# Performance work log

Hardware: AMD Instinct MI355X
Metric: run time of the kernel (lower is better)

## Reference

```python
import jax, jax.numpy as jnp
import numpy as np
import math

B, Q_LEN, PAST, HID = 1, 1024, 3072, 4096
NH, NKV, HD = 32, 8, 128
KV_LEN = PAST + Q_LEN
ROPE_THETA = 10000.0


def setup_inputs() -> dict:
    key = jax.random.key(0)
    ks = jax.random.split(key, 8)
    s = 0.02
    hidden_states = jax.random.normal(ks[0], (B, Q_LEN, HID), jnp.float32)
    # additive causal mask with KV cache offset: query i attends keys j <= PAST + i
    i = jnp.arange(Q_LEN)[:, None]
    j = jnp.arange(KV_LEN)[None, :]
    attention_mask = jnp.where(j <= PAST + i, 0.0, -1e9).astype(jnp.float32)[None, None]
    position_ids = (jnp.arange(Q_LEN, dtype=jnp.int64) + PAST)[None, :]
    past_k = jax.random.normal(ks[1], (B, NKV, PAST, HD), jnp.float32)
    past_v = jax.random.normal(ks[2], (B, NKV, PAST, HD), jnp.float32)
    Wq = jax.random.normal(ks[3], (NH * HD, HID), jnp.float32) * s
    Wk = jax.random.normal(ks[4], (NKV * HD, HID), jnp.float32) * s
    Wv = jax.random.normal(ks[5], (NKV * HD, HID), jnp.float32) * s
    Wo = jax.random.normal(ks[6], (HID, NH * HD), jnp.float32) * s
    return {"hidden_states": hidden_states, "attention_mask": attention_mask,
            "position_ids": position_ids, "past_k": past_k, "past_v": past_v,
            "Wq": Wq, "Wk": Wk, "Wv": Wv, "Wo": Wo}


def _rope_tables(seq_len, head_dim, dtype):
    inv_freq = 1.0 / (ROPE_THETA ** (jnp.arange(0, head_dim, 2, dtype=jnp.float32) / head_dim))
    t = jnp.arange(seq_len, dtype=jnp.float32)
    freqs = jnp.outer(t, inv_freq)            # [seq, hd/2]
    emb = jnp.concatenate([freqs, freqs], -1)  # [seq, hd]
    return jnp.cos(emb).astype(dtype), jnp.sin(emb).astype(dtype)


def _rotate_half(x):
    x1, x2 = jnp.split(x, 2, axis=-1)
    return jnp.concatenate([-x2, x1], axis=-1)


def reference(hidden_states, attention_mask, position_ids, past_k, past_v, Wq, Wk, Wv, Wo):
    bsz, q_len, _ = hidden_states.shape
    q = (hidden_states @ Wq.T).reshape(bsz, q_len, NH, HD).transpose(0, 2, 1, 3)
    k = (hidden_states @ Wk.T).reshape(bsz, q_len, NKV, HD).transpose(0, 2, 1, 3)
    v = (hidden_states @ Wv.T).reshape(bsz, q_len, NKV, HD).transpose(0, 2, 1, 3)

    kv_seq_len = q_len + past_k.shape[2]
    cos_t, sin_t = _rope_tables(kv_seq_len, HD, q.dtype)
    cos = cos_t[position_ids][:, None]  # [b,1,q,hd]
    sin = sin_t[position_ids][:, None]
    q = q * cos + _rotate_half(q) * sin
    k = k * cos + _rotate_half(k) * sin

    k = jnp.concatenate([past_k, k], axis=2)  # [b,nkv,kv,hd]
    v = jnp.concatenate([past_v, v], axis=2)
    n_rep = NH // NKV
    k = jnp.repeat(k, n_rep, axis=1)  # GQA repeat_kv -> [b,nh,kv,hd]
    v = jnp.repeat(v, n_rep, axis=1)

    scores = jnp.einsum('bhqd,bhkd->bhqk', q, k) / math.sqrt(HD)
    scores = scores + attention_mask
    weights = jax.nn.softmax(scores.astype(jnp.float32), axis=-1).astype(q.dtype)
    attn = jnp.einsum('bhqk,bhkd->bhqd', weights, v)
    attn = attn.transpose(0, 2, 1, 3).reshape(bsz, q_len, NH * HD)
    return attn @ Wo.T
```

## Files before the change

### kernel.cpp

```cpp
#include <hip/hip_runtime.h>

#define QLEN 1024
#define PASTN 3072
#define KVLEN 4096
#define HIDN 4096
#define NHEAD 32
#define NKVH 8
#define HDIM 128
#define NQKVC 6144

typedef unsigned short u16;
typedef __bf16 bf16x8 __attribute__((ext_vector_type(8)));
typedef float f32x4 __attribute__((ext_vector_type(4)));
typedef u16 us8 __attribute__((ext_vector_type(8)));
typedef u16 us4 __attribute__((ext_vector_type(4)));

__device__ __forceinline__ u16 f2bf(float x) {
  unsigned u = __builtin_bit_cast(unsigned, x);
  u += 0x7fffu + ((u >> 16) & 1u);
  return (u16)(u >> 16);
}
__device__ __forceinline__ float bf2f(u16 b) {
  return __builtin_bit_cast(float, (unsigned)b << 16);
}

#define GLL16(gp, lp) __builtin_amdgcn_global_load_lds( \
    (const __attribute__((address_space(1))) void*)(gp), \
    (__attribute__((address_space(3))) void*)(lp), 16, 0, 0)

__global__ __launch_bounds__(256) void cvt_kernel(const float* __restrict__ src,
                                                  u16* __restrict__ dst, int n) {
  int i = (blockIdx.x * 256 + threadIdx.x) * 4;
  if (i >= n) return;
  float4 f = *(const float4*)(src + i);
  ushort4 o = make_ushort4(f2bf(f.x), f2bf(f.y), f2bf(f.z), f2bf(f.w));
  *(ushort4*)(dst + i) = o;
}

__device__ __forceinline__ void storeC(float* p, float v) { *p = v; }
__device__ __forceinline__ void storeC(u16* p, float v) { *p = f2bf(v); }

template <typename CT>
__global__ __launch_bounds__(256) void gemm_bt(const u16* __restrict__ A,
                                               const u16* __restrict__ B,
                                               CT* __restrict__ C, int M, int N, int K) {
  __shared__ u16 Alds[2][128 * 32];
  __shared__ u16 Blds[2][128 * 32];
  const int tid = threadIdx.x, wid = tid >> 6, lane = tid & 63;
  const int m0 = blockIdx.y * 128, n0 = blockIdx.x * 128;
  const int wm = (wid >> 1) * 64, wn = (wid & 1) * 64;
  const int l15 = lane & 15, l4 = lane >> 4;
  const int srow = lane >> 2, scol = (lane & 3) * 8;
  f32x4 acc[4][4] = {};
  auto stage = [&](int buf, int kt) {
#pragma unroll
    for (int i = 0; i < 2; ++i) {
      int c = wid * 2 + i;
      GLL16(A + (size_t)(m0 + c * 16 + srow) * K + kt + scol, &Alds[buf][c * 512]);
      GLL16(B + (size_t)(n0 + c * 16 + srow) * K + kt + scol, &Blds[buf][c * 512]);
    }
  };
  stage(0, 0);
  __syncthreads();
  int cur = 0;
  for (int kt = 0; kt < K; kt += 32) {
    if (kt + 32 < K) stage(cur ^ 1, kt + 32);
    bf16x8 a[4], b[4];
#pragma unroll
    for (int i = 0; i < 4; ++i) {
      a[i] = *(const bf16x8*)&Alds[cur][(wm + i * 16 + l15) * 32 + l4 * 8];
      b[i] = *(const bf16x8*)&Blds[cur][(wn + i * 16 + l15) * 32 + l4 * 8];
    }
#pragma unroll
    for (int i = 0; i < 4; ++i)
#pragma unroll
      for (int j = 0; j < 4; ++j)
        acc[i][j] = __builtin_amdgcn_mfma_f32_16x16x32_bf16(a[i], b[j], acc[i][j], 0, 0, 0);
    __syncthreads();
    cur ^= 1;
  }
#pragma unroll
  for (int i = 0; i < 4; ++i)
#pragma unroll
    for (int j = 0; j < 4; ++j) {
      int row = m0 + wm + i * 16 + l4 * 4;
      int col = n0 + wn + j * 16 + l15;
#pragma unroll
      for (int r = 0; r < 4; ++r) storeC(&C[(size_t)(row + r) * N + col], acc[i][j][r]);
    }
}

__global__ __launch_bounds__(256) void rope_q_kernel(const u16* __restrict__ qkv,
                                                     u16* __restrict__ qr) {
  int idx = blockIdx.x * 256 + threadIdx.x;
  int i = idx & 63, h = (idx >> 6) & 31, r = idx >> 11;
  float freq = __expf(-(float)i * (9.210340371976184f / 64.f));
  float angle = (float)(PASTN + r) * freq;
  float sn, cs;
  sincosf(angle, &sn, &cs);
  int base = r * NQKVC + h * HDIM + i;
  float x1 = bf2f(qkv[base]);
  float x2 = bf2f(qkv[base + 64]);
  int ob = r * HIDN + h * HDIM + i;
  qr[ob] = f2bf(x1 * cs - x2 * sn);
  qr[ob + 64] = f2bf(x2 * cs + x1 * sn);
}

__global__ __launch_bounds__(256) void repack_k_kernel(const float* __restrict__ past_k,
                                                       const u16* __restrict__ qkv,
                                                       u16* __restrict__ kb) {
  int idx = blockIdx.x * 256 + threadIdx.x;
  int d = idx & 127, kv = (idx >> 7) & 4095, hk = idx >> 19;
  float val;
  if (kv < PASTN) {
    val = past_k[((size_t)hk * PASTN + kv) * HDIM + d];
  } else {
    int r = kv - PASTN;
    float x = bf2f(qkv[(size_t)r * NQKVC + 4096 + hk * HDIM + d]);
    float xp = bf2f(qkv[(size_t)r * NQKVC + 4096 + hk * HDIM + (d ^ 64)]);
    int i = d & 63;
    float freq = __expf(-(float)i * (9.210340371976184f / 64.f));
    float angle = (float)(PASTN + r) * freq;
    float sn, cs;
    sincosf(angle, &sn, &cs);
    val = (d < 64) ? (x * cs - xp * sn) : (x * cs + xp * sn);
  }
  kb[idx] = f2bf(val);
}

__global__ __launch_bounds__(256) void repack_vt_kernel(const float* __restrict__ past_v,
                                                        const u16* __restrict__ qkv,
                                                        u16* __restrict__ vtb) {
  __shared__ u16 tile[32][136];
  int hk = blockIdx.y, kv0 = blockIdx.x * 32, tid = threadIdx.x;
  int j = tid >> 3, d0 = (tid & 7) * 16;
  if (kv0 < PASTN) {
    const float* src = past_v + ((size_t)hk * PASTN + kv0 + j) * HDIM + d0;
#pragma unroll
    for (int x = 0; x < 16; x += 4) {
      float4 f = *(const float4*)(src + x);
      tile[j][d0 + x] = f2bf(f.x);
      tile[j][d0 + x + 1] = f2bf(f.y);
      tile[j][d0 + x + 2] = f2bf(f.z);
      tile[j][d0 + x + 3] = f2bf(f.w);
    }
  } else {
    int r = kv0 - PASTN + j;
    const u16* src = qkv + (size_t)r * NQKVC + 5120 + hk * HDIM + d0;
    *(us8*)&tile[j][d0] = *(const us8*)src;
    *(us8*)&tile[j][d0 + 8] = *(const us8*)(src + 8);
  }
  __syncthreads();
  int d = tid >> 1, jb = (tid & 1) * 16;
  us8 o0, o1;
#pragma unroll
  for (int x = 0; x < 8; ++x) {
    o0[x] = tile[jb + x][d];
    o1[x] = tile[jb + 8 + x][d];
  }
  u16* dst = vtb + ((size_t)hk * HDIM + d) * KVLEN + kv0 + jb;
  *(us8*)dst = o0;
  *(us8*)(dst + 8) = o1;
}

__global__ __launch_bounds__(256) void attn_kernel(const u16* __restrict__ q,
                                                   const u16* __restrict__ kc,
                                                   const u16* __restrict__ vt,
                                                   u16* __restrict__ o) {
  __shared__ u16 Klds[2][64 * 128];
  __shared__ u16 Vlds[2][128 * 64];
  const int tid = threadIdx.x, wid = tid >> 6, lane = tid & 63;
  const int l15 = lane & 15, l4 = lane >> 4;
  const int h = blockIdx.y, hk = h >> 2;
  const int q0 = blockIdx.x * 64;
  bf16x8 qf[4];
  {
    const u16* qp = q + (size_t)(q0 + wid * 16 + l15) * HIDN + h * HDIM + l4 * 8;
#pragma unroll
    for (int dk = 0; dk < 4; ++dk) qf[dk] = *(const bf16x8*)(qp + dk * 32);
  }
  float m_run = -1e30f, l_run = 0.f;
  f32x4 oacc[8] = {};
  const u16* kbase = kc + (size_t)hk * KVLEN * HDIM;
  const u16* vbase = vt + (size_t)hk * HDIM * KVLEN;
  const int ntiles = (PASTN + q0 + 64) >> 6;
  const float C = 0.12753102f;
  const int qpos = PASTN + q0 + wid * 16 + l15;
  auto stage = [&](int buf, int kv0) {
#pragma unroll
    for (int i = 0; i < 4; ++i) {
      const int base = (wid * 4 + i) * 512;
      const int row = (wid * 4 + i) * 4 + l4;
      const int kap = (row & 0x23) | ((row & 0x0C) << 1) | ((row & 0x10) >> 2);
      const int col = l15 ^ (row & 7);
      GLL16(kbase + (size_t)(kv0 + kap) * HDIM + col * 8, &Klds[buf][base]);
    }
#pragma unroll
    for (int i = 0; i < 4; ++i) {
      const int base = (wid * 4 + i) * 512;
      const int d = (wid * 4 + i) * 8 + (lane >> 3);
      const int kvo = ((lane & 7) ^ (d & 7)) * 8;
      GLL16(vbase + (size_t)d * KVLEN + kv0 + kvo, &Vlds[buf][base]);
    }
  };
  stage(0, 0);
  __syncthreads();
  int cur = 0;
  for (int t = 0; t < ntiles; ++t) {
    if (t + 1 < ntiles) stage(cur ^ 1, (t + 1) << 6);
    const int kv0 = t << 6;
    const u16* Kb = Klds[cur];
    const u16* Vb = Vlds[cur];
    f32x4 s[4];
    __builtin_amdgcn_s_setprio(1);
#pragma unroll
    for (int kj = 0; kj < 4; ++kj) {
      s[kj] = f32x4{0.f, 0.f, 0.f, 0.f};
#pragma unroll
      for (int dk = 0; dk < 4; ++dk) {
        const int idx = (kj * 16 + l15) * 128 + ((dk * 32 + l4 * 8) ^ ((l15 & 7) << 3));
        bf16x8 kf = *(const bf16x8*)&Kb[idx];
        s[kj] = __builtin_amdgcn_mfma_f32_16x16x32_bf16(kf, qf[dk], s[kj], 0, 0, 0);
      }
    }
    __builtin_amdgcn_s_setprio(0);
    float pm = -1e30f;
    if (t == ntiles - 1) {
#pragma unroll
      for (int kj = 0; kj < 4; ++kj) {
        const int kb = kv0 + ((kj >> 1) << 5) + l4 * 8 + ((kj & 1) << 2);
#pragma unroll
        for (int r = 0; r < 4; ++r) {
          float v = s[kj][r] * C;
          if (kb + r > qpos) v = -1e30f;
          s[kj][r] = v;
          pm = fmaxf(pm, v);
        }
      }
    } else {
#pragma unroll
      for (int kj = 0; kj < 4; ++kj)
#pragma unroll
        for (int r = 0; r < 4; ++r) {
          float v = s[kj][r] * C;
          s[kj][r] = v;
          pm = fmaxf(pm, v);
        }
    }
    pm = fmaxf(pm, __shfl_xor(pm, 16));
    pm = fmaxf(pm, __shfl_xor(pm, 32));
    if (!__all(pm <= m_run)) {
      const float mn = fmaxf(m_run, pm);
      const float corr = exp2f(m_run - mn);
      m_run = mn;
      l_run *= corr;
#pragma unroll
      for (int di = 0; di < 8; ++di)
#pragma unroll
        for (int r = 0; r < 4; ++r) oacc[di][r] *= corr;
    }
    float rs = 0.f;
#pragma unroll
    for (int kj = 0; kj < 4; ++kj)
#pragma unroll
      for (int r = 0; r < 4; ++r) {
        const float p = exp2f(s[kj][r] - m_run);
        s[kj][r] = p;
        rs += p;
      }
    rs += __shfl_xor(rs, 16);
    rs += __shfl_xor(rs, 32);
    l_run += rs;
    __builtin_amdgcn_s_setprio(1);
#pragma unroll
    for (int b = 0; b < 2; ++b) {
      bf16x8 pa;
#pragma unroll
      for (int r = 0; r < 4; ++r) {
        pa[r] = (__bf16)s[2 * b][r];
        pa[4 + r] = (__bf16)s[2 * b + 1][r];
      }
#pragma unroll
      for (int di = 0; di < 8; ++di) {
        const int d = di * 16 + l15;
        const int idx = d * 64 + ((b * 32 + l4 * 8) ^ ((d & 7) << 3));
        bf16x8 vf = *(const bf16x8*)&Vb[idx];
        oacc[di] = __builtin_amdgcn_mfma_f32_16x16x32_bf16(vf, pa, oacc[di], 0, 0, 0);
      }
    }
    __builtin_amdgcn_s_setprio(0);
    __syncthreads();
    cur ^= 1;
  }
  const float inv = 1.f / l_run;
  u16* Kb0 = Klds[0];
#pragma unroll
  for (int di = 0; di < 8; ++di) {
    us4 w4;
#pragma unroll
    for (int r = 0; r < 4; ++r) w4[r] = f2bf(oacc[di][r] * inv);
    const int row = wid * 16 + l15;
    *(us4*)&Kb0[row * 128 + ((di * 16 + l4 * 4) ^ ((l15 & 7) << 3))] = w4;
  }
  __syncthreads();
  {
    const int row = tid >> 2, c0 = (tid & 3) * 32;
    u16* dst = o + (size_t)(q0 + row) * HIDN + h * HDIM + c0;
#pragma unroll
    for (int x = 0; x < 4; ++x)
      *(us8*)(dst + x * 8) =
          *(const us8*)&Kb0[row * 128 + ((c0 + x * 8) ^ ((row & 7) << 3))];
  }
}

extern "C" void kernel_launch(void* const* d_in, const int* in_sizes, int n_in,
                              void* d_out, int out_size, void* d_ws, size_t ws_size,
                              hipStream_t stream) {
  (void)in_sizes; (void)n_in; (void)out_size; (void)ws_size;
  const float* hidden = (const float*)d_in[0];
  const float* past_k = (const float*)d_in[3];
  const float* past_v = (const float*)d_in[4];
  const float* Wq = (const float*)d_in[5];
  const float* Wk = (const float*)d_in[6];
  const float* Wv = (const float*)d_in[7];
  const float* Wo = (const float*)d_in[8];
  float* out = (float*)d_out;

  char* w = (char*)d_ws;
  u16* hiddenb = (u16*)w; w += (size_t)QLEN * HIDN * 2;
  u16* wqkv    = (u16*)w; w += (size_t)NQKVC * HIDN * 2;
  u16* wo      = (u16*)w; w += (size_t)HIDN * HIDN * 2;
  u16* qkvraw  = (u16*)w; w += (size_t)QLEN * NQKVC * 2;
  u16* qrope   = (u16*)w; w += (size_t)QLEN * HIDN * 2;
  u16* kbuf    = (u16*)w; w += (size_t)NKVH * KVLEN * HDIM * 2;
  u16* vtbuf   = (u16*)w; w += (size_t)NKVH * HDIM * KVLEN * 2;
  u16* attnb   = (u16*)w; w += (size_t)QLEN * HIDN * 2;

  cvt_kernel<<<(QLEN * HIDN) / 1024, 256, 0, stream>>>(hidden, hiddenb, QLEN * HIDN);
  cvt_kernel<<<(NHEAD * HDIM * HIDN) / 1024, 256, 0, stream>>>(Wq, wqkv, NHEAD * HDIM * HIDN);
  cvt_kernel<<<(NKVH * HDIM * HIDN) / 1024, 256, 0, stream>>>(Wk, wqkv + (size_t)4096 * HIDN,
                                                              NKVH * HDIM * HIDN);
  cvt_kernel<<<(NKVH * HDIM * HIDN) / 1024, 256, 0, stream>>>(Wv, wqkv + (size_t)5120 * HIDN,
                                                              NKVH * HDIM * HIDN);
  cvt_kernel<<<(HIDN * HIDN) / 1024, 256, 0, stream>>>(Wo, wo, HIDN * HIDN);

  gemm_bt<u16><<<dim3(NQKVC / 128, QLEN / 128), 256, 0, stream>>>(hiddenb, wqkv, qkvraw,
                                                                  QLEN, NQKVC, HIDN);

  rope_q_kernel<<<(QLEN * NHEAD * 64) / 256, 256, 0, stream>>>(qkvraw, qrope);
  repack_k_kernel<<<(NKVH * KVLEN * HDIM) / 256, 256, 0, stream>>>(past_k, qkvraw, kbuf);
  repack_vt_kernel<<<dim3(KVLEN / 32, NKVH), 256, 0, stream>>>(past_v, qkvraw, vtbuf);

  attn_kernel<<<dim3(QLEN / 64, NHEAD), 256, 0, stream>>>(qrope, kbuf, vtbuf, attnb);

  gemm_bt<float><<<dim3(HIDN / 128, QLEN / 128), 256, 0, stream>>>(attnb, wo, out,
                                                                   QLEN, HIDN, HIDN);
}
```

Before: 375.6 us.

## Switch attention to 32x32x16 MFMA with two waves per 64-query block

The attention kernel now uses 32x32x16 bf16 MFMA instructions instead of 16x16x32, so each wave owns 32 query rows, and the block shrinks from four waves to two (128 threads). The LDS swizzle for K and V staging and for the output tile is redone to fit the new fragment layouts, and one cross-lane shuffle step in the softmax reductions goes away. The aim is fewer LDS fragment reads per FLOP and fewer MFMA issues. In exchange, each block has half as many waves to hide latency, each thread issues twice as many staging loads, and register pressure per thread is higher.

```diff
diff --git a/kernel.cpp b/kernel.cpp
--- a/kernel.cpp
+++ b/kernel.cpp
@@ -12,6 +12,7 @@
 typedef unsigned short u16;
 typedef __bf16 bf16x8 __attribute__((ext_vector_type(8)));
 typedef float f32x4 __attribute__((ext_vector_type(4)));
+typedef float f32x16 __attribute__((ext_vector_type(16)));
 typedef u16 us8 __attribute__((ext_vector_type(8)));
 typedef u16 us4 __attribute__((ext_vector_type(4)));
 
@@ -163,44 +164,45 @@
   *(us8*)(dst + 8) = o1;
 }
 
-__global__ __launch_bounds__(256) void attn_kernel(const u16* __restrict__ q,
+__global__ __launch_bounds__(128) void attn_kernel(const u16* __restrict__ q,
                                                    const u16* __restrict__ kc,
                                                    const u16* __restrict__ vt,
                                                    u16* __restrict__ o) {
   __shared__ u16 Klds[2][64 * 128];
   __shared__ u16 Vlds[2][128 * 64];
   const int tid = threadIdx.x, wid = tid >> 6, lane = tid & 63;
-  const int l15 = lane & 15, l4 = lane >> 4;
+  const int l31 = lane & 31, hi = lane >> 5, l15 = lane & 15;
   const int h = blockIdx.y, hk = h >> 2;
   const int q0 = blockIdx.x * 64;
-  bf16x8 qf[4];
+  const int qrow = q0 + wid * 32 + l31;
+  bf16x8 qf[8];
   {
-    const u16* qp = q + (size_t)(q0 + wid * 16 + l15) * HIDN + h * HDIM + l4 * 8;
-#pragma unroll
-    for (int dk = 0; dk < 4; ++dk) qf[dk] = *(const bf16x8*)(qp + dk * 32);
+    const u16* qp = q + (size_t)qrow * HIDN + h * HDIM + hi * 8;
+#pragma unroll
+    for (int dk = 0; dk < 8; ++dk) qf[dk] = *(const bf16x8*)(qp + dk * 16);
   }
   float m_run = -1e30f, l_run = 0.f;
-  f32x4 oacc[8] = {};
+  f32x16 oacc[4] = {};
   const u16* kbase = kc + (size_t)hk * KVLEN * HDIM;
   const u16* vbase = vt + (size_t)hk * HDIM * KVLEN;
   const int ntiles = (PASTN + q0 + 64) >> 6;
   const float C = 0.12753102f;
-  const int qpos = PASTN + q0 + wid * 16 + l15;
+  const int qpos = PASTN + qrow;
   auto stage = [&](int buf, int kv0) {
 #pragma unroll
-    for (int i = 0; i < 4; ++i) {
-      const int base = (wid * 4 + i) * 512;
-      const int row = (wid * 4 + i) * 4 + l4;
-      const int kap = (row & 0x23) | ((row & 0x0C) << 1) | ((row & 0x10) >> 2);
-      const int col = l15 ^ (row & 7);
-      GLL16(kbase + (size_t)(kv0 + kap) * HDIM + col * 8, &Klds[buf][base]);
-    }
-#pragma unroll
-    for (int i = 0; i < 4; ++i) {
-      const int base = (wid * 4 + i) * 512;
-      const int d = (wid * 4 + i) * 8 + (lane >> 3);
-      const int kvo = ((lane & 7) ^ (d & 7)) * 8;
-      GLL16(vbase + (size_t)d * KVLEN + kv0 + kvo, &Vlds[buf][base]);
+    for (int i = 0; i < 8; ++i) {
+      const int w = wid * 8 + i;
+      const int p = w * 4 + (lane >> 4);
+      const int key = (p & 0x33) | ((p & 4) << 1) | ((p & 8) >> 1);
+      const int sl = (lane & 15) ^ (p & 15);
+      GLL16(kbase + (size_t)(kv0 + key) * HDIM + sl * 8, &Klds[buf][w * 512]);
+    }
+#pragma unroll
+    for (int i = 0; i < 8; ++i) {
+      const int w = wid * 8 + i;
+      const int d = w * 8 + (lane >> 3);
+      const int sl = (lane & 7) ^ ((lane >> 3) & 7);
+      GLL16(vbase + (size_t)d * KVLEN + kv0 + sl * 8, &Vlds[buf][w * 512]);
     }
   };
   stage(0, 0);
@@ -211,43 +213,39 @@
     const int kv0 = t << 6;
     const u16* Kb = Klds[cur];
     const u16* Vb = Vlds[cur];
-    f32x4 s[4];
+    f32x16 s[2] = {};
     __builtin_amdgcn_s_setprio(1);
 #pragma unroll
-    for (int kj = 0; kj < 4; ++kj) {
-      s[kj] = f32x4{0.f, 0.f, 0.f, 0.f};
-#pragma unroll
-      for (int dk = 0; dk < 4; ++dk) {
-        const int idx = (kj * 16 + l15) * 128 + ((dk * 32 + l4 * 8) ^ ((l15 & 7) << 3));
+    for (int tt = 0; tt < 2; ++tt)
+#pragma unroll
+      for (int dk = 0; dk < 8; ++dk) {
+        const int idx = (tt * 32 + l31) * 128 + (((dk * 2 + hi) ^ l15) * 8);
         bf16x8 kf = *(const bf16x8*)&Kb[idx];
-        s[kj] = __builtin_amdgcn_mfma_f32_16x16x32_bf16(kf, qf[dk], s[kj], 0, 0, 0);
+        s[tt] = __builtin_amdgcn_mfma_f32_32x32x16_bf16(kf, qf[dk], s[tt], 0, 0, 0);
       }
-    }
     __builtin_amdgcn_s_setprio(0);
     float pm = -1e30f;
     if (t == ntiles - 1) {
 #pragma unroll
-      for (int kj = 0; kj < 4; ++kj) {
-        const int kb = kv0 + ((kj >> 1) << 5) + l4 * 8 + ((kj & 1) << 2);
-#pragma unroll
-        for (int r = 0; r < 4; ++r) {
-          float v = s[kj][r] * C;
-          if (kb + r > qpos) v = -1e30f;
-          s[kj][r] = v;
+      for (int tt = 0; tt < 2; ++tt)
+#pragma unroll
+        for (int reg = 0; reg < 16; ++reg) {
+          const int key = kv0 + tt * 32 + (reg & 7) + 8 * hi + ((reg & 8) << 1);
+          float v = s[tt][reg] * C;
+          if (key > qpos) v = -1e30f;
+          s[tt][reg] = v;
           pm = fmaxf(pm, v);
         }
-      }
     } else {
 #pragma unroll
-      for (int kj = 0; kj < 4; ++kj)
-#pragma unroll
-        for (int r = 0; r < 4; ++r) {
-          float v = s[kj][r] * C;
-          s[kj][r] = v;
+      for (int tt = 0; tt < 2; ++tt)
+#pragma unroll
+        for (int reg = 0; reg < 16; ++reg) {
+          float v = s[tt][reg] * C;
+          s[tt][reg] = v;
           pm = fmaxf(pm, v);
         }
     }
-    pm = fmaxf(pm, __shfl_xor(pm, 16));
     pm = fmaxf(pm, __shfl_xor(pm, 32));
     if (!__all(pm <= m_run)) {
       const float mn = fmaxf(m_run, pm);
@@ -255,37 +253,32 @@
       m_run = mn;
       l_run *= corr;
 #pragma unroll
-      for (int di = 0; di < 8; ++di)
-#pragma unroll
-        for (int r = 0; r < 4; ++r) oacc[di][r] *= corr;
+      for (int db = 0; db < 4; ++db)
+#pragma unroll
+        for (int r = 0; r < 16; ++r) oacc[db][r] *= corr;
     }
     float rs = 0.f;
 #pragma unroll
-    for (int kj = 0; kj < 4; ++kj)
-#pragma unroll
-      for (int r = 0; r < 4; ++r) {
-        const float p = exp2f(s[kj][r] - m_run);
-        s[kj][r] = p;
+    for (int tt = 0; tt < 2; ++tt)
+#pragma unroll
+      for (int reg = 0; reg < 16; ++reg) {
+        const float p = exp2f(s[tt][reg] - m_run);
+        s[tt][reg] = p;
         rs += p;
       }
-    rs += __shfl_xor(rs, 16);
     rs += __shfl_xor(rs, 32);
     l_run += rs;
     __builtin_amdgcn_s_setprio(1);
 #pragma unroll
-    for (int b = 0; b < 2; ++b) {
+    for (int kc2 = 0; kc2 < 4; ++kc2) {
       bf16x8 pa;
 #pragma unroll
-      for (int r = 0; r < 4; ++r) {
-        pa[r] = (__bf16)s[2 * b][r];
-        pa[4 + r] = (__bf16)s[2 * b + 1][r];
-      }
-#pragma unroll
-      for (int di = 0; di < 8; ++di) {
-        const int d = di * 16 + l15;
-        const int idx = d * 64 + ((b * 32 + l4 * 8) ^ ((d & 7) << 3));
+      for (int j = 0; j < 8; ++j) pa[j] = (__bf16)s[kc2 >> 1][(kc2 & 1) * 8 + j];
+#pragma unroll
+      for (int db = 0; db < 4; ++db) {
+        const int idx = (db * 32 + l31) * 64 + (((kc2 * 2 + hi) ^ (l31 & 7)) * 8);
         bf16x8 vf = *(const bf16x8*)&Vb[idx];
-        oacc[di] = __builtin_amdgcn_mfma_f32_16x16x32_bf16(vf, pa, oacc[di], 0, 0, 0);
+        oacc[db] = __builtin_amdgcn_mfma_f32_32x32x16_bf16(vf, pa, oacc[db], 0, 0, 0);
       }
     }
     __builtin_amdgcn_s_setprio(0);
@@ -293,23 +286,25 @@
     cur ^= 1;
   }
   const float inv = 1.f / l_run;
-  u16* Kb0 = Klds[0];
-#pragma unroll
-  for (int di = 0; di < 8; ++di) {
-    us4 w4;
-#pragma unroll
-    for (int r = 0; r < 4; ++r) w4[r] = f2bf(oacc[di][r] * inv);
-    const int row = wid * 16 + l15;
-    *(us4*)&Kb0[row * 128 + ((di * 16 + l4 * 4) ^ ((l15 & 7) << 3))] = w4;
-  }
+  u16* Olds = &Klds[0][0];
+  const int orow = wid * 32 + l31;
+#pragma unroll
+  for (int db = 0; db < 4; ++db)
+#pragma unroll
+    for (int g = 0; g < 4; ++g) {
+      us4 w4;
+#pragma unroll
+      for (int j = 0; j < 4; ++j) w4[j] = f2bf(oacc[db][g * 4 + j] * inv);
+      const int s16 = (db * 4 + g) ^ (orow & 15);
+      *(us4*)&Olds[orow * 128 + s16 * 8 + hi * 4] = w4;
+    }
   __syncthreads();
-  {
-    const int row = tid >> 2, c0 = (tid & 3) * 32;
-    u16* dst = o + (size_t)(q0 + row) * HIDN + h * HDIM + c0;
-#pragma unroll
-    for (int x = 0; x < 4; ++x)
-      *(us8*)(dst + x * 8) =
-          *(const us8*)&Kb0[row * 128 + ((c0 + x * 8) ^ ((row & 7) << 3))];
+#pragma unroll
+  for (int x = 0; x < 8; ++x) {
+    const int row = x * 8 + (tid >> 4);
+    const int sl = tid & 15;
+    us8 v = *(const us8*)&Olds[row * 128 + ((sl ^ (row & 15)) << 3)];
+    *(us8*)(o + (size_t)(q0 + row) * HIDN + h * HDIM + sl * 8) = v;
   }
 }
 
@@ -351,7 +346,7 @@
   repack_k_kernel<<<(NKVH * KVLEN * HDIM) / 256, 256, 0, stream>>>(past_k, qkvraw, kbuf);
   repack_vt_kernel<<<dim3(KVLEN / 32, NKVH), 256, 0, stream>>>(past_v, qkvraw, vtbuf);
 
-  attn_kernel<<<dim3(QLEN / 64, NHEAD), 256, 0, stream>>>(qrope, kbuf, vtbuf, attnb);
+  attn_kernel<<<dim3(QLEN / 64, NHEAD), 128, 0, stream>>>(qrope, kbuf, vtbuf, attnb);
 
   gemm_bt<float><<<dim3(HIDN / 128, QLEN / 128), 256, 0, stream>>>(attnb, wo, out,
                                                                    QLEN, HIDN, HIDN);
```

After: 394.2 us. 5.0% more time.
